# Kernel tuning notes

Measured on AMD Instinct MI355X. Metric: run time of the kernel, lower is better.

## Reference

```python
import jax, jax.numpy as jnp
import numpy as np

H = 2048      # hidden_size
NH = 16       # num_attention_heads
HD = H // NH  # head_dim = 128
B, S = 2, 2048
ROPE_BASE = 10000.0


def setup_inputs() -> dict:
    key = jax.random.key(0)
    ks = jax.random.split(key, 9)
    init = 0.02
    inp = {
        "hidden_states": jax.random.normal(ks[0], (B, S, H), dtype=jnp.float32),
        # torch nn.Linear weights are [out_features, in_features]
        "wq": jax.random.normal(ks[1], (H, H), dtype=jnp.float32) * init,
        "bq": jnp.zeros((H,), dtype=jnp.float32),
        "wk": jax.random.normal(ks[2], (H, H), dtype=jnp.float32) * init,
        "bk": jnp.zeros((H,), dtype=jnp.float32),
        "wv": jax.random.normal(ks[3], (H, H), dtype=jnp.float32) * init,
        "bv": jnp.zeros((H,), dtype=jnp.float32),
        "wo": jax.random.normal(ks[4], (H, H), dtype=jnp.float32) * init,
        "bo": jnp.zeros((H,), dtype=jnp.float32),
    }
    return inp


def _rope_cos_sin(seq_len, dim, dtype):
    # standard RoPE tables: [seq_len, dim]
    inv_freq = 1.0 / (ROPE_BASE ** (jnp.arange(0, dim, 2, dtype=jnp.float32) / dim))
    freqs = jnp.arange(seq_len, dtype=jnp.float32)[:, None] * inv_freq[None, :]
    emb = jnp.concatenate([freqs, freqs], axis=-1)  # [S, dim]
    return jnp.cos(emb).astype(dtype), jnp.sin(emb).astype(dtype)


def _rotate_half(x):
    half = x.shape[-1] // 2
    return jnp.concatenate([-x[..., half:], x[..., :half]], axis=-1)


def reference(hidden_states, wq, bq, wk, bk, wv, bv, wo, bo):
    b, s, h = hidden_states.shape
    scale = HD ** -0.5

    def proj(x, w, bias):
        y = jnp.einsum("bsh,oh->bso", x, w) + bias
        # -> [b, nh, s, hd]
        return y.reshape(b, s, NH, HD).transpose(0, 2, 1, 3)

    q = proj(hidden_states, wq, bq)
    k = proj(hidden_states, wk, bk)
    v = proj(hidden_states, wv, bv)

    # rotary embeddings on q, k
    cos, sin = _rope_cos_sin(s, HD, q.dtype)  # [s, hd]
    q = q * cos + _rotate_half(q) * sin
    k = k * cos + _rotate_half(k) * sin

    # causal additive mask [s, s]
    mask = jnp.triu(jnp.full((s, s), -1e9, dtype=q.dtype), k=1)

    scores = jnp.einsum("bhqd,bhkd->bhqk", q, k) * scale + mask
    probs = jax.nn.softmax(scores, axis=-1)
    attn = jnp.einsum("bhqk,bhkd->bhqd", probs, v)
    attn = attn.transpose(0, 2, 1, 3).reshape(b, s, h)
    out = jnp.einsum("bsh,oh->bso", attn, wo) + bo
    return out
```

## Files before the change

kernel.cpp:

```cpp
#include <hip/hip_runtime.h>

typedef unsigned short u16;
typedef __attribute__((ext_vector_type(8))) __bf16 bf16x8;
typedef __attribute__((ext_vector_type(4))) float f32x4;
typedef __attribute__((ext_vector_type(4))) u16 u16x4;
typedef __attribute__((ext_vector_type(8))) u16 u16x8;

constexpr int S = 2048;
constexpr int H = 2048;
constexpr int NH = 16;
constexpr int HD = 128;
constexpr int M = 4096;
constexpr float SCALE = 0.08838834764831845f;

__device__ __forceinline__ u16 f2bf(float f) {
  union { float f; unsigned u; } v; v.f = f;
  unsigned r = v.u + 0x7fffu + ((v.u >> 16) & 1u);
  return (u16)(r >> 16);
}
__device__ __forceinline__ float bf2f(u16 u) {
  union { unsigned u; float f; } v; v.u = ((unsigned)u) << 16;
  return v.f;
}
__device__ __forceinline__ unsigned cvt_pk_bf16(float lo, float hi) {
  unsigned r;
  asm("v_cvt_pk_bf16_f32 %0, %1, %2" : "=v"(r) : "v"(lo), "v"(hi));
  return r;
}
__device__ __forceinline__ f32x4 MFMA16(bf16x8 a, bf16x8 b, f32x4 c) {
  return __builtin_amdgcn_mfma_f32_16x16x32_bf16(a, b, c, 0, 0, 0);
}

__device__ __forceinline__ void gld16(const u16* g, u16* l) {
  __builtin_amdgcn_global_load_lds(
      (const __attribute__((address_space(1))) void*)g,
      (__attribute__((address_space(3))) void*)l, 16, 0, 0);
}

#define SBAR  { __builtin_amdgcn_sched_barrier(0); __builtin_amdgcn_s_barrier(); __builtin_amdgcn_sched_barrier(0); }
#define LGKM0 { asm volatile("s_waitcnt lgkmcnt(0)" ::: "memory"); __builtin_amdgcn_sched_barrier(0); }

__global__ __launch_bounds__(256) void cast_kernel(const float* __restrict__ in,
                                                   u16* __restrict__ out, int n) {
  int i = (blockIdx.x * 256 + threadIdx.x) * 4;
  if (i >= n) return;
  float4 v = *(const float4*)(in + i);
  u16x4 o;
  o[0] = f2bf(v.x); o[1] = f2bf(v.y); o[2] = f2bf(v.z); o[3] = f2bf(v.w);
  *(u16x4*)(out + i) = o;
}

__global__ __launch_bounds__(256) void cast4_kernel(const float* __restrict__ i0,
                                                    const float* __restrict__ i1,
                                                    const float* __restrict__ i2,
                                                    const float* __restrict__ i3,
                                                    u16* o0, u16* o1, u16* o2, u16* o3) {
  const float* in; u16* out;
  switch (blockIdx.y) {
    case 0: in = i0; out = o0; break;
    case 1: in = i1; out = o1; break;
    case 2: in = i2; out = o2; break;
    default: in = i3; out = o3; break;
  }
  int i = (blockIdx.x * 256 + threadIdx.x) * 4;
  float4 v = *(const float4*)(in + i);
  u16x4 o;
  o[0] = f2bf(v.x); o[1] = f2bf(v.y); o[2] = f2bf(v.z); o[3] = f2bf(v.w);
  *(u16x4*)(out + i) = o;
}

__global__ __launch_bounds__(256) void concat_bias_k(const float* __restrict__ bq,
                                                     const float* __restrict__ bk,
                                                     const float* __restrict__ bv,
                                                     float* __restrict__ bqkv) {
  int i = blockIdx.x * 256 + threadIdx.x;
  const float* src = (i < 2048) ? bq : (i < 4096) ? bk : bv;
  bqkv[i] = src[i & 2047];
}

__global__ __launch_bounds__(256) void rope_table_k(float* __restrict__ tab) {
  int i = blockIdx.x * 256 + threadIdx.x;
  if (i >= S * 64) return;
  int s = i >> 6, d = i & 63;
  float freq = expf(-(float)d * (9.210340371976184f / 64.f));
  float ang = (float)s * freq;
  tab[i * 2]     = cosf(ang);
  tab[i * 2 + 1] = sinf(ang);
}

__global__ __launch_bounds__(256) void rope_apply2_k(u16* __restrict__ Qb, u16* __restrict__ Kb,
                                                     const float* __restrict__ tab) {
  u16* X = blockIdx.y ? Kb : Qb;
  const float sc = blockIdx.y ? 1.f : SCALE;
  int i = blockIdx.x * 256 + threadIdx.x;
  int j0 = (i & 7) * 8;
  int h  = (i >> 3) & 15;
  int m  = i >> 7;
  int s  = m & (S - 1);
  u16* p = X + (size_t)m * H + h * HD;
  u16x8 lo = *(u16x8*)(p + j0);
  u16x8 hi = *(u16x8*)(p + 64 + j0);
  u16x8 nlo, nhi;
  const float* tb = tab + ((size_t)s * 64 + j0) * 2;
  #pragma unroll
  for (int j = 0; j < 8; ++j) {
    float c = tb[j * 2], sn = tb[j * 2 + 1];
    float xl = bf2f(lo[j]), xh = bf2f(hi[j]);
    nlo[j] = f2bf((xl * c - xh * sn) * sc);
    nhi[j] = f2bf((xh * c + xl * sn) * sc);
  }
  *(u16x8*)(p + j0) = nlo;
  *(u16x8*)(p + 64 + j0) = nhi;
}

template<int NW, int EMODE>
__device__ __forceinline__ void gemm_body(const u16* __restrict__ A,
                                          const u16* __restrict__ Bw,
                                          const float* __restrict__ bias,
                                          void* __restrict__ out0, void* __restrict__ out1,
                                          void* __restrict__ out2,
                                          int brow, int bcol,
                                          u16* AsL, u16* BsL) {
  const int t = threadIdx.x;
  const int w = t >> 6, l = t & 63;
  const int wr = w >> 2, wc = w & 3;
  const int lr = l & 15, lg = l >> 4;
  const int swz = lr & 7;

  f32x4 acc[8][NW] = {};
  bf16x8 af[4], b0[NW], b1[NW];

  const int sr = t >> 3, sj = t & 7;

  auto STAGE_A = [&](int BUF, int HALF, int TILE) {
    u16* d = AsL + BUF * (256 * 64) + HALF * (128 * 64);
    const u16* sp = A + (size_t)(brow + HALF * 128) * H + TILE * 64;
    gld16(sp + (size_t)sr * H        + ((sj ^ (sr & 7)) * 8), d + t * 8);
    gld16(sp + (size_t)(64 + sr) * H + ((sj ^ (sr & 7)) * 8), d + (512 + t) * 8);
  };
  auto STAGE_B = [&](int BUF, int TILE) {
    u16* d = BsL + BUF * (NW * 64 * 64);
    const u16* sp = Bw + (size_t)bcol * H + TILE * 64;
    #pragma unroll
    for (int i = 0; i < NW; ++i)
      gld16(sp + (size_t)(i * 64 + sr) * H + ((sj ^ (sr & 7)) * 8),
            d + (i * 512 + t) * 8);
  };
  auto LDA = [&](int BUF, int KH, int MB) {
    const u16* base = AsL + BUF * (256 * 64) + (wr * 128 + MB * 16 + lr) * 64;
    #pragma unroll
    for (int i = 0; i < 4; ++i)
      af[i] = *(const bf16x8*)(base + i * (16 * 64) + (((KH * 4 + lg) ^ swz) * 8));
  };
  auto LDB = [&](int BUF, int KH, bf16x8* bb) {
    const u16* base = BsL + BUF * (NW * 64 * 64) + (wc * (NW * 16) + lr) * 64;
    #pragma unroll
    for (int n = 0; n < NW; ++n)
      bb[n] = *(const bf16x8*)(base + n * (16 * 64) + (((KH * 4 + lg) ^ swz) * 8));
  };
  auto MM = [&](int MB, bf16x8* bb) {
    __builtin_amdgcn_s_setprio(1);
    #pragma unroll
    for (int i = 0; i < 4; ++i)
      #pragma unroll
      for (int n = 0; n < NW; ++n)
        acc[MB + i][n] = MFMA16(af[i], bb[n], acc[MB + i][n]);
    __builtin_amdgcn_s_setprio(0);
  };
  auto GATE = [&]() {
    if constexpr (NW == 3) { asm volatile("s_waitcnt vmcnt(3)" ::: "memory"); }
    else                   { asm volatile("s_waitcnt vmcnt(2)" ::: "memory"); }
  };

  STAGE_A(0, 0, 0); STAGE_A(0, 1, 0);
  STAGE_B(0, 0);
  STAGE_B(1, 1);
  GATE();
  SBAR;

  for (int J = 0; J < 16; ++J) {
    const int u = 2 * J;
    const bool more = (J < 15);
    LDA(0, 0, 0); LDB(0, 0, b0);
    STAGE_A(1, 0, u + 1);
    SBAR; LGKM0; MM(0, b0); SBAR;
    LDA(0, 0, 4);
    STAGE_A(1, 1, u + 1);
    SBAR; LGKM0; MM(4, b0); SBAR;
    LDA(0, 1, 0); LDB(0, 1, b1);
    SBAR; LGKM0; MM(0, b1); SBAR;
    LDA(0, 1, 4);
    if (more) STAGE_B(0, u + 2);
    SBAR; LGKM0; MM(4, b1);
    if (more) { GATE(); } else { asm volatile("s_waitcnt vmcnt(0)" ::: "memory"); }
    SBAR;
    LDA(1, 0, 0); LDB(1, 0, b0);
    if (more) STAGE_A(0, 0, u + 2);
    SBAR; LGKM0; MM(0, b0); SBAR;
    LDA(1, 0, 4);
    if (more) STAGE_A(0, 1, u + 2);
    SBAR; LGKM0; MM(4, b0); SBAR;
    LDA(1, 1, 0); LDB(1, 1, b1);
    SBAR; LGKM0; MM(0, b1); SBAR;
    LDA(1, 1, 4);
    if (more) STAGE_B(1, u + 3);
    SBAR; LGKM0; MM(4, b1);
    if (more) { GATE(); SBAR; }
  }

  #pragma unroll
  for (int m = 0; m < 8; ++m) {
    const int row0 = brow + wr * 128 + m * 16 + lg * 4;
    #pragma unroll
    for (int n = 0; n < NW; ++n) {
      const int gcol0 = bcol + wc * (NW * 16) + n * 16;
      const float bv = bias[gcol0 + lr];
      if constexpr (EMODE == 0) {
        float* C = (float*)out0;
        #pragma unroll
        for (int r = 0; r < 4; ++r)
          C[(size_t)(row0 + r) * H + gcol0 + lr] = acc[m][n][r] + bv;
      } else {
        const int sel = gcol0 >> 11;
        const int col = (gcol0 & 2047) + lr;
        if (sel < 2) {
          u16* C = sel ? (u16*)out1 : (u16*)out0;
          #pragma unroll
          for (int r = 0; r < 4; ++r)
            C[(size_t)(row0 + r) * H + col] = f2bf(acc[m][n][r] + bv);
        } else {
          const int hh = col >> 7, d = col & 127;
          const int b = row0 >> 11, s0 = row0 & (S - 1);
          u16x4 pk;
          #pragma unroll
          for (int r = 0; r < 4; ++r) pk[r] = f2bf(acc[m][n][r] + bv);
          *(u16x4*)((u16*)out2 + ((size_t)((b * 16 + hh) * 128 + d)) * S + s0) = pk;
        }
      }
    }
  }
}

__global__ __launch_bounds__(512, 2) void gemm_qkv8(const u16* __restrict__ xb,
                                                    const u16* __restrict__ wqkv,
                                                    const float* __restrict__ bqkv,
                                                    u16* Qb, u16* Kb, u16* Vt) {
  __shared__ u16 AsL[2 * 256 * 64];
  __shared__ u16 BsL[2 * 192 * 64];
  const int id = blockIdx.x;
  const int xcd = id & 7, sid = id >> 3;
  const int bx = xcd * 4 + (sid & 3), by = sid >> 2;
  gemm_body<3, 3>(xb, wqkv, bqkv, Qb, Kb, Vt, by * 256, bx * 192, AsL, BsL);
}

__global__ __launch_bounds__(512, 2) void gemm_o8(const u16* __restrict__ A,
                                                  const u16* __restrict__ W,
                                                  const float* __restrict__ bias,
                                                  float* __restrict__ C) {
  __shared__ u16 AsL[2 * 256 * 64];
  __shared__ u16 BsL[2 * 128 * 64];
  const int id = blockIdx.x;
  const int xcd = id & 7, sid = id >> 3;
  const int bx = xcd * 2 + (sid & 1), by = sid >> 1;
  gemm_body<2, 0>(A, W, bias, C, nullptr, nullptr, by * 256, bx * 128, AsL, BsL);
}

__global__ __launch_bounds__(256) void attn_fwd(const u16* __restrict__ Q,
                                                const u16* __restrict__ Kx,
                                                const u16* __restrict__ Vt,
                                                u16* __restrict__ O) {
  const int id = blockIdx.x;
  const int xcd = id & 7, slot = id >> 3;
  const int bh = (slot >> 4) * 8 + xcd;
  const int pid = slot & 15;
  const int b = bh >> 4, h = bh & 15;
  const int t = threadIdx.x, w = t >> 6, l = t & 63;
  const int lr = l & 15, lg = l >> 4;
  const int swz = lr & 7;

  __shared__ u16 Ks[2][64 * 128];
  __shared__ u16 Vs[2][128 * 64];
  __shared__ u16 P_lds[4][16 * 64];
  u16* pw = &P_lds[w][0];

  const u16* kbase = Kx + (size_t)(b * S) * H + h * HD;
  const u16* vbase = Vt + (size_t)bh * HD * S;

  auto stageK = [&](int bf, int k0) {
    #pragma unroll
    for (int it = 0; it < 4; ++it) {
      int c = it * 256 + t;
      int row = c >> 4, j = c & 15;
      gld16(kbase + (size_t)(k0 + row) * H + ((j ^ (row & 7)) * 8), &Ks[bf][0] + c * 8);
    }
  };
  auto stageV = [&](int bf, int k0) {
    #pragma unroll
    for (int it = 0; it < 4; ++it) {
      int c = it * 256 + t;
      int row = c >> 3, j = c & 7;
      gld16(vbase + (size_t)row * S + k0 + ((j ^ (row & 7)) * 8), &Vs[bf][0] + c * 8);
    }
  };

  int cur = 0;
  for (int qi = 0; qi < 2; ++qi) {
    const int qt = qi ? pid : (31 - pid);
    const int q0 = qt * 64 + w * 16;

    bf16x8 qa[4];
    const u16* qbase = Q + (size_t)(b * S + q0 + lr) * H + h * HD;
    #pragma unroll
    for (int ks = 0; ks < 4; ++ks)
      qa[ks] = *(const bf16x8*)(qbase + ks * 32 + lg * 8);

    f32x4 acc[8] = {};
    float mrun[4], lrun[4];
    #pragma unroll
    for (int r = 0; r < 4; ++r) { mrun[r] = -1e30f; lrun[r] = 0.f; }

    __syncthreads();
    stageK(cur, 0);
    stageV(cur, 0);
    __syncthreads();

    for (int kt = 0; kt <= qt; ++kt) {
      if (kt < qt) {
        stageK(cur ^ 1, (kt + 1) * 64);
        stageV(cur ^ 1, (kt + 1) * 64);
      }
      const u16* kl = &Ks[cur][0];
      const u16* vl = &Vs[cur][0];

      f32x4 sc[4] = {};
      __builtin_amdgcn_s_setprio(1);
      #pragma unroll
      for (int ks = 0; ks < 4; ++ks) {
        #pragma unroll
        for (int f = 0; f < 4; ++f) {
          bf16x8 kf = *(const bf16x8*)(kl + (f * 16 + lr) * 128 + (((ks * 4 + lg) ^ swz) * 8));
          sc[f] = __builtin_amdgcn_mfma_f32_16x16x32_bf16(qa[ks], kf, sc[f], 0, 0, 0);
        }
      }
      __builtin_amdgcn_s_setprio(0);
      const bool diag = (kt == qt);
      float p[4][4];
      #pragma unroll
      for (int f = 0; f < 4; ++f)
        #pragma unroll
        for (int r = 0; r < 4; ++r) {
          float v = sc[f][r];
          if (diag && (f * 16 + lr > w * 16 + lg * 4 + r)) v = -1e30f;
          p[f][r] = v;
        }
      float mx[4];
      #pragma unroll
      for (int r = 0; r < 4; ++r) {
        float m0 = fmaxf(fmaxf(p[0][r], p[1][r]), fmaxf(p[2][r], p[3][r]));
        m0 = fmaxf(m0, __shfl_xor(m0, 1));
        m0 = fmaxf(m0, __shfl_xor(m0, 2));
        m0 = fmaxf(m0, __shfl_xor(m0, 4));
        m0 = fmaxf(m0, __shfl_xor(m0, 8));
        mx[r] = m0;
      }
      bool grow = (mx[0] > mrun[0] + 8.f) || (mx[1] > mrun[1] + 8.f) ||
                  (mx[2] > mrun[2] + 8.f) || (mx[3] > mrun[3] + 8.f);
      if (__any(grow)) {
        float resc[4];
        #pragma unroll
        for (int r = 0; r < 4; ++r) {
          float mnew = fmaxf(mrun[r], mx[r]);
          resc[r] = __expf(mrun[r] - mnew);
          mrun[r] = mnew;
          lrun[r] *= resc[r];
        }
        #pragma unroll
        for (int fd = 0; fd < 8; ++fd) {
          f32x4 a = acc[fd];
          a[0] *= resc[0]; a[1] *= resc[1]; a[2] *= resc[2]; a[3] *= resc[3];
          acc[fd] = a;
        }
      }
      #pragma unroll
      for (int r = 0; r < 4; ++r) {
        float sum = 0.f;
        #pragma unroll
        for (int f = 0; f < 4; ++f) {
          float e = __expf(p[f][r] - mrun[r]);
          p[f][r] = e;
          sum += e;
        }
        sum += __shfl_xor(sum, 1);
        sum += __shfl_xor(sum, 2);
        sum += __shfl_xor(sum, 4);
        sum += __shfl_xor(sum, 8);
        lrun[r] += sum;
      }
      {
        const int r0 = lg * 4;
        #pragma unroll
        for (int f = 0; f < 4; ++f) {
          const int col = f * 16 + lr;
          unsigned w01 = cvt_pk_bf16(p[f][0], p[f][1]);
          unsigned w23 = cvt_pk_bf16(p[f][2], p[f][3]);
          pw[(r0 + 0) * 64 + (col ^ (((r0 + 0) & 7) << 3))] = (u16)(w01 & 0xffffu);
          pw[(r0 + 1) * 64 + (col ^ (((r0 + 1) & 7) << 3))] = (u16)(w01 >> 16);
          pw[(r0 + 2) * 64 + (col ^ (((r0 + 2) & 7) << 3))] = (u16)(w23 & 0xffffu);
          pw[(r0 + 3) * 64 + (col ^ (((r0 + 3) & 7) << 3))] = (u16)(w23 >> 16);
        }
      }
      __builtin_amdgcn_s_setprio(1);
      #pragma unroll
      for (int ks = 0; ks < 2; ++ks) {
        int col0 = ks * 32 + lg * 8;
        bf16x8 pa = *(const bf16x8*)(pw + lr * 64 + (col0 ^ (swz << 3)));
        #pragma unroll
        for (int fd = 0; fd < 8; ++fd) {
          bf16x8 vb = *(const bf16x8*)(vl + (fd * 16 + lr) * 64 + (((ks * 4 + lg) ^ swz) * 8));
          acc[fd] = __builtin_amdgcn_mfma_f32_16x16x32_bf16(pa, vb, acc[fd], 0, 0, 0);
        }
      }
      __builtin_amdgcn_s_setprio(0);
      __syncthreads();
      cur ^= 1;
    }

    u16* ob = O + (size_t)(b * S + q0 + lg * 4) * H + h * HD;
    #pragma unroll
    for (int r = 0; r < 4; ++r) {
      float inv = 1.f / lrun[r];
      #pragma unroll
      for (int fd = 0; fd < 8; ++fd)
        ob[(size_t)r * H + fd * 16 + lr] = f2bf(acc[fd][r] * inv);
    }
  }
}

extern "C" void kernel_launch(void* const* d_in, const int* in_sizes, int n_in,
                              void* d_out, int out_size, void* d_ws, size_t ws_size,
                              hipStream_t stream) {
  const float* x  = (const float*)d_in[0];
  const float* wq = (const float*)d_in[1];
  const float* bq = (const float*)d_in[2];
  const float* wk = (const float*)d_in[3];
  const float* bk = (const float*)d_in[4];
  const float* wv = (const float*)d_in[5];
  const float* bv = (const float*)d_in[6];
  const float* wo = (const float*)d_in[7];
  const float* bo = (const float*)d_in[8];

  char* ws = (char*)d_ws;
  u16*   xb    = (u16*)(ws);
  u16*   wqkvb = (u16*)(ws + (16ull << 20));
  u16*   wob   = (u16*)(ws + (40ull << 20));
  u16*   Qb    = (u16*)(ws + (48ull << 20));
  u16*   Kb    = (u16*)(ws + (64ull << 20));
  u16*   Vt    = (u16*)(ws + (80ull << 20));
  u16*   Ob    = (u16*)(ws + (96ull << 20));
  float* tab   = (float*)(ws + (112ull << 20));
  float* bqkv  = (float*)(ws + (113ull << 20));

  cast_kernel<<<M * H / 1024, 256, 0, stream>>>(x, xb, M * H);
  cast4_kernel<<<dim3(H * H / 1024, 4), 256, 0, stream>>>(
      wq, wk, wv, wo, wqkvb, wqkvb + (size_t)H * H, wqkvb + 2ull * H * H, wob);
  rope_table_k<<<(S * 64 + 255) / 256, 256, 0, stream>>>(tab);
  concat_bias_k<<<24, 256, 0, stream>>>(bq, bk, bv, bqkv);

  gemm_qkv8<<<512, 512, 0, stream>>>(xb, wqkvb, bqkv, Qb, Kb, Vt);

  rope_apply2_k<<<dim3(M * NH * 8 / 256, 2), 256, 0, stream>>>(Qb, Kb, tab);

  attn_fwd<<<512, 256, 0, stream>>>(Qb, Kb, Vt, Ob);

  gemm_o8<<<256, 512, 0, stream>>>(Ob, wob, bo, (float*)d_out);
}
```

Before: 275.5 us.

## Replace 256-row GEMMs with simpler 128x128 tiles and fuse RoPE into QKV epilogue

Replaces the hand-scheduled 256xN, 512-thread GEMM body (fine-grained barriers, split staging, vmcnt gating) with a plain double-buffered 128x128 tile GEMM using 256 threads. Both the QKV and output projections switch to the smaller tiles and larger grids. RoPE and the Q scale move into the QKV GEMM epilogue, which exchanges the rotate-half partner columns through LDS, so the separate rope pass over Q and K is dropped. The cost is a simpler pipeline with less compute/load overlap, smaller tiles with less data reuse, and extra LDS round trips in the epilogue.

Result: no change. 280.0 us (+1.6%).

```diff
diff --git a/kernel.cpp b/kernel.cpp
--- a/kernel.cpp
+++ b/kernel.cpp
@@ -37,8 +37,7 @@
       (__attribute__((address_space(3))) void*)l, 16, 0, 0);
 }
 
-#define SBAR  { __builtin_amdgcn_sched_barrier(0); __builtin_amdgcn_s_barrier(); __builtin_amdgcn_sched_barrier(0); }
-#define LGKM0 { asm volatile("s_waitcnt lgkmcnt(0)" ::: "memory"); __builtin_amdgcn_sched_barrier(0); }
+#define BAR  __builtin_amdgcn_s_barrier()
 
 __global__ __launch_bounds__(256) void cast_kernel(const float* __restrict__ in,
                                                    u16* __restrict__ out, int n) {
@@ -88,181 +87,174 @@
   tab[i * 2 + 1] = sinf(ang);
 }
 
-__global__ __launch_bounds__(256) void rope_apply2_k(u16* __restrict__ Qb, u16* __restrict__ Kb,
-                                                     const float* __restrict__ tab) {
-  u16* X = blockIdx.y ? Kb : Qb;
-  const float sc = blockIdx.y ? 1.f : SCALE;
-  int i = blockIdx.x * 256 + threadIdx.x;
-  int j0 = (i & 7) * 8;
-  int h  = (i >> 3) & 15;
-  int m  = i >> 7;
-  int s  = m & (S - 1);
-  u16* p = X + (size_t)m * H + h * HD;
-  u16x8 lo = *(u16x8*)(p + j0);
-  u16x8 hi = *(u16x8*)(p + 64 + j0);
-  u16x8 nlo, nhi;
-  const float* tb = tab + ((size_t)s * 64 + j0) * 2;
-  #pragma unroll
-  for (int j = 0; j < 8; ++j) {
-    float c = tb[j * 2], sn = tb[j * 2 + 1];
-    float xl = bf2f(lo[j]), xh = bf2f(hi[j]);
-    nlo[j] = f2bf((xl * c - xh * sn) * sc);
-    nhi[j] = f2bf((xh * c + xl * sn) * sc);
-  }
-  *(u16x8*)(p + j0) = nlo;
-  *(u16x8*)(p + 64 + j0) = nhi;
-}
-
-template<int NW, int EMODE>
-__device__ __forceinline__ void gemm_body(const u16* __restrict__ A,
-                                          const u16* __restrict__ Bw,
-                                          const float* __restrict__ bias,
-                                          void* __restrict__ out0, void* __restrict__ out1,
-                                          void* __restrict__ out2,
-                                          int brow, int bcol,
-                                          u16* AsL, u16* BsL) {
+template<int EMODE>
+__device__ __forceinline__ void gemm128(const u16* __restrict__ A,
+                                        const u16* __restrict__ Bw,
+                                        const float* __restrict__ bias,
+                                        const float* __restrict__ tab,
+                                        void* __restrict__ out0, void* __restrict__ out1,
+                                        void* __restrict__ out2,
+                                        int brow, int bcol,
+                                        u16* AsL, u16* BsL) {
   const int t = threadIdx.x;
   const int w = t >> 6, l = t & 63;
-  const int wr = w >> 2, wc = w & 3;
+  const int wr = w >> 1, wc = w & 1;
   const int lr = l & 15, lg = l >> 4;
   const int swz = lr & 7;
 
-  f32x4 acc[8][NW] = {};
-  bf16x8 af[4], b0[NW], b1[NW];
+  f32x4 acc[4][4] = {};
 
   const int sr = t >> 3, sj = t & 7;
 
-  auto STAGE_A = [&](int BUF, int HALF, int TILE) {
-    u16* d = AsL + BUF * (256 * 64) + HALF * (128 * 64);
-    const u16* sp = A + (size_t)(brow + HALF * 128) * H + TILE * 64;
-    gld16(sp + (size_t)sr * H        + ((sj ^ (sr & 7)) * 8), d + t * 8);
-    gld16(sp + (size_t)(64 + sr) * H + ((sj ^ (sr & 7)) * 8), d + (512 + t) * 8);
-  };
-  auto STAGE_B = [&](int BUF, int TILE) {
-    u16* d = BsL + BUF * (NW * 64 * 64);
-    const u16* sp = Bw + (size_t)bcol * H + TILE * 64;
-    #pragma unroll
-    for (int i = 0; i < NW; ++i)
-      gld16(sp + (size_t)(i * 64 + sr) * H + ((sj ^ (sr & 7)) * 8),
-            d + (i * 512 + t) * 8);
-  };
-  auto LDA = [&](int BUF, int KH, int MB) {
-    const u16* base = AsL + BUF * (256 * 64) + (wr * 128 + MB * 16 + lr) * 64;
+  auto STAGE = [&](int BUF, int TILE) {
+    u16* da = AsL + BUF * (128 * 64);
+    const u16* sa = A + (size_t)brow * H + TILE * 64;
+    #pragma unroll
+    for (int it = 0; it < 4; ++it) {
+      int row = it * 32 + sr;
+      gld16(sa + (size_t)row * H + ((sj ^ (row & 7)) * 8), da + (it * 256 + t) * 8);
+    }
+    u16* db = BsL + BUF * (128 * 64);
+    const u16* sb = Bw + (size_t)bcol * H + TILE * 64;
+    #pragma unroll
+    for (int it = 0; it < 4; ++it) {
+      int row = it * 32 + sr;
+      gld16(sb + (size_t)row * H + ((sj ^ (row & 7)) * 8), db + (it * 256 + t) * 8);
+    }
+  };
+  auto LDA = [&](int BUF, int KH, bf16x8* aa) {
+    const u16* base = AsL + BUF * (128 * 64) + (wr * 64 + lr) * 64;
     #pragma unroll
     for (int i = 0; i < 4; ++i)
-      af[i] = *(const bf16x8*)(base + i * (16 * 64) + (((KH * 4 + lg) ^ swz) * 8));
+      aa[i] = *(const bf16x8*)(base + i * (16 * 64) + (((KH * 4 + lg) ^ swz) * 8));
   };
   auto LDB = [&](int BUF, int KH, bf16x8* bb) {
-    const u16* base = BsL + BUF * (NW * 64 * 64) + (wc * (NW * 16) + lr) * 64;
-    #pragma unroll
-    for (int n = 0; n < NW; ++n)
+    const u16* base = BsL + BUF * (128 * 64) + (wc * 64 + lr) * 64;
+    #pragma unroll
+    for (int n = 0; n < 4; ++n)
       bb[n] = *(const bf16x8*)(base + n * (16 * 64) + (((KH * 4 + lg) ^ swz) * 8));
   };
-  auto MM = [&](int MB, bf16x8* bb) {
+  auto MM = [&](bf16x8* aa, bf16x8* bb) {
     __builtin_amdgcn_s_setprio(1);
     #pragma unroll
     for (int i = 0; i < 4; ++i)
       #pragma unroll
-      for (int n = 0; n < NW; ++n)
-        acc[MB + i][n] = MFMA16(af[i], bb[n], acc[MB + i][n]);
+      for (int n = 0; n < 4; ++n)
+        acc[i][n] = MFMA16(aa[i], bb[n], acc[i][n]);
     __builtin_amdgcn_s_setprio(0);
   };
-  auto GATE = [&]() {
-    if constexpr (NW == 3) { asm volatile("s_waitcnt vmcnt(3)" ::: "memory"); }
-    else                   { asm volatile("s_waitcnt vmcnt(2)" ::: "memory"); }
-  };
-
-  STAGE_A(0, 0, 0); STAGE_A(0, 1, 0);
-  STAGE_B(0, 0);
-  STAGE_B(1, 1);
-  GATE();
-  SBAR;
-
-  for (int J = 0; J < 16; ++J) {
-    const int u = 2 * J;
-    const bool more = (J < 15);
-    LDA(0, 0, 0); LDB(0, 0, b0);
-    STAGE_A(1, 0, u + 1);
-    SBAR; LGKM0; MM(0, b0); SBAR;
-    LDA(0, 0, 4);
-    STAGE_A(1, 1, u + 1);
-    SBAR; LGKM0; MM(4, b0); SBAR;
-    LDA(0, 1, 0); LDB(0, 1, b1);
-    SBAR; LGKM0; MM(0, b1); SBAR;
-    LDA(0, 1, 4);
-    if (more) STAGE_B(0, u + 2);
-    SBAR; LGKM0; MM(4, b1);
-    if (more) { GATE(); } else { asm volatile("s_waitcnt vmcnt(0)" ::: "memory"); }
-    SBAR;
-    LDA(1, 0, 0); LDB(1, 0, b0);
-    if (more) STAGE_A(0, 0, u + 2);
-    SBAR; LGKM0; MM(0, b0); SBAR;
-    LDA(1, 0, 4);
-    if (more) STAGE_A(0, 1, u + 2);
-    SBAR; LGKM0; MM(4, b0); SBAR;
-    LDA(1, 1, 0); LDB(1, 1, b1);
-    SBAR; LGKM0; MM(0, b1); SBAR;
-    LDA(1, 1, 4);
-    if (more) STAGE_B(1, u + 3);
-    SBAR; LGKM0; MM(4, b1);
-    if (more) { GATE(); SBAR; }
+
+  STAGE(0, 0);
+  asm volatile("s_waitcnt vmcnt(0)" ::: "memory");
+  BAR;
+
+  int c = 0;
+  for (int u = 0; u < 32; ++u) {
+    if (u < 31) STAGE(c ^ 1, u + 1);
+    bf16x8 aa[4], bb[4];
+    LDA(c, 0, aa); LDB(c, 0, bb); MM(aa, bb);
+    LDA(c, 1, aa); LDB(c, 1, bb); MM(aa, bb);
+    asm volatile("s_waitcnt vmcnt(0)" ::: "memory");
+    BAR;
+    c ^= 1;
   }
 
-  #pragma unroll
-  for (int m = 0; m < 8; ++m) {
-    const int row0 = brow + wr * 128 + m * 16 + lg * 4;
-    #pragma unroll
-    for (int n = 0; n < NW; ++n) {
-      const int gcol0 = bcol + wc * (NW * 16) + n * 16;
-      const float bv = bias[gcol0 + lr];
-      if constexpr (EMODE == 0) {
-        float* C = (float*)out0;
+  if constexpr (EMODE == 0) {
+    float* C = (float*)out0;
+    #pragma unroll
+    for (int m = 0; m < 4; ++m) {
+      const int row0 = brow + wr * 64 + m * 16 + lg * 4;
+      #pragma unroll
+      for (int n = 0; n < 4; ++n) {
+        const int col = bcol + wc * 64 + n * 16 + lr;
+        const float bv = bias[col];
         #pragma unroll
         for (int r = 0; r < 4; ++r)
-          C[(size_t)(row0 + r) * H + gcol0 + lr] = acc[m][n][r] + bv;
-      } else {
-        const int sel = gcol0 >> 11;
-        const int col = (gcol0 & 2047) + lr;
-        if (sel < 2) {
-          u16* C = sel ? (u16*)out1 : (u16*)out0;
+          C[(size_t)(row0 + r) * H + col] = acc[m][n][r] + bv;
+      }
+    }
+  } else {
+    const int sel = bcol >> 11;
+    if (sel < 2) {
+      float* lf = (float*)AsL;
+      u16* Cq = sel ? (u16*)out1 : (u16*)out0;
+      const float scl = sel ? 1.f : SCALE;
+      #pragma unroll
+      for (int m = 0; m < 4; ++m) {
+        __syncthreads();
+        float mine[4][4];
+        #pragma unroll
+        for (int n = 0; n < 4; ++n) {
+          const float bv = bias[bcol + wc * 64 + n * 16 + lr];
           #pragma unroll
-          for (int r = 0; r < 4; ++r)
-            C[(size_t)(row0 + r) * H + col] = f2bf(acc[m][n][r] + bv);
-        } else {
+          for (int r = 0; r < 4; ++r) {
+            mine[n][r] = acc[m][n][r] + bv;
+            lf[w * (16 * 66) + (lg * 4 + r) * 66 + n * 16 + lr] = mine[n][r];
+          }
+        }
+        __syncthreads();
+        #pragma unroll
+        for (int n = 0; n < 4; ++n) {
+          const int j = n * 16 + lr;
+          const int hcol = (bcol & 2047) + wc * 64 + j;
+          #pragma unroll
+          for (int r = 0; r < 4; ++r) {
+            const int row = brow + wr * 64 + m * 16 + lg * 4 + r;
+            const int s = row & (S - 1);
+            float pr = lf[(w ^ 1) * (16 * 66) + (lg * 4 + r) * 66 + j];
+            float2 cs = ((const float2*)tab)[s * 64 + j];
+            float out = wc ? (mine[n][r] * cs.x + pr * cs.y)
+                           : (mine[n][r] * cs.x - pr * cs.y);
+            Cq[(size_t)row * H + hcol] = f2bf(out * scl);
+          }
+        }
+      }
+    } else {
+      u16* Vt = (u16*)out2;
+      #pragma unroll
+      for (int m = 0; m < 4; ++m) {
+        const int row0 = brow + wr * 64 + m * 16 + lg * 4;
+        #pragma unroll
+        for (int n = 0; n < 4; ++n) {
+          const int col = (bcol & 2047) + wc * 64 + n * 16 + lr;
+          const float bv = bias[bcol + wc * 64 + n * 16 + lr];
           const int hh = col >> 7, d = col & 127;
           const int b = row0 >> 11, s0 = row0 & (S - 1);
           u16x4 pk;
           #pragma unroll
           for (int r = 0; r < 4; ++r) pk[r] = f2bf(acc[m][n][r] + bv);
-          *(u16x4*)((u16*)out2 + ((size_t)((b * 16 + hh) * 128 + d)) * S + s0) = pk;
+          *(u16x4*)(Vt + ((size_t)((b * 16 + hh) * 128 + d)) * S + s0) = pk;
         }
       }
     }
   }
 }
 
-__global__ __launch_bounds__(512, 2) void gemm_qkv8(const u16* __restrict__ xb,
+__global__ __launch_bounds__(256, 2) void gemm_qkv2(const u16* __restrict__ xb,
                                                     const u16* __restrict__ wqkv,
                                                     const float* __restrict__ bqkv,
+                                                    const float* __restrict__ tab,
                                                     u16* Qb, u16* Kb, u16* Vt) {
-  __shared__ u16 AsL[2 * 256 * 64];
-  __shared__ u16 BsL[2 * 192 * 64];
+  __shared__ u16 AsL[2 * 128 * 64];
+  __shared__ u16 BsL[2 * 128 * 64];
   const int id = blockIdx.x;
   const int xcd = id & 7, sid = id >> 3;
-  const int bx = xcd * 4 + (sid & 3), by = sid >> 2;
-  gemm_body<3, 3>(xb, wqkv, bqkv, Qb, Kb, Vt, by * 256, bx * 192, AsL, BsL);
-}
-
-__global__ __launch_bounds__(512, 2) void gemm_o8(const u16* __restrict__ A,
+  const int bx = xcd * 6 + (sid % 6);
+  const int by = sid / 6;
+  gemm128<3>(xb, wqkv, bqkv, tab, Qb, Kb, Vt, by * 128, bx * 128, AsL, BsL);
+}
+
+__global__ __launch_bounds__(256, 2) void gemm_o2(const u16* __restrict__ A,
                                                   const u16* __restrict__ W,
                                                   const float* __restrict__ bias,
                                                   float* __restrict__ C) {
-  __shared__ u16 AsL[2 * 256 * 64];
+  __shared__ u16 AsL[2 * 128 * 64];
   __shared__ u16 BsL[2 * 128 * 64];
   const int id = blockIdx.x;
   const int xcd = id & 7, sid = id >> 3;
-  const int bx = xcd * 2 + (sid & 1), by = sid >> 1;
-  gemm_body<2, 0>(A, W, bias, C, nullptr, nullptr, by * 256, bx * 128, AsL, BsL);
+  const int bx = xcd * 2 + (sid & 1);
+  const int by = sid >> 1;
+  gemm128<0>(A, W, bias, nullptr, C, nullptr, nullptr, by * 128, bx * 128, AsL, BsL);
 }
 
 __global__ __launch_bounds__(256) void attn_fwd(const u16* __restrict__ Q,
@@ -466,11 +458,9 @@
   rope_table_k<<<(S * 64 + 255) / 256, 256, 0, stream>>>(tab);
   concat_bias_k<<<24, 256, 0, stream>>>(bq, bk, bv, bqkv);
 
-  gemm_qkv8<<<512, 512, 0, stream>>>(xb, wqkvb, bqkv, Qb, Kb, Vt);
-
-  rope_apply2_k<<<dim3(M * NH * 8 / 256, 2), 256, 0, stream>>>(Qb, Kb, tab);
+  gemm_qkv2<<<1536, 256, 0, stream>>>(xb, wqkvb, bqkv, tab, Qb, Kb, Vt);
 
   attn_fwd<<<512, 256, 0, stream>>>(Qb, Kb, Vt, Ob);
 
-  gemm_o8<<<256, 512, 0, stream>>>(Ob, wob, bo, (float*)d_out);
-}
+  gemm_o2<<<512, 256, 0, stream>>>(Ob, wob, bo, (float*)d_out);
+}
```
